# Performance work log

Hardware: AMD Instinct MI355X
Metric: run time of the kernel (lower is better)

Reference implementation:

```python
import jax, jax.numpy as jnp
import numpy as np

D = 2        # dof (input_dim of fc1)
H1 = 64      # hidden width
N = 262144   # batch
NEG_SLOPE = -0.01  # NOTE: original uses self.neg_slope=-0.01 in the analytic derivative
                   # while the forward activation uses F.leaky_relu default slope +0.01.
                   # We replicate this exactly.

def _lin_init(k, out_d, in_d):
    bound = 1.0 / np.sqrt(in_d)
    kw, kb = jax.random.split(k)
    W = jax.random.uniform(kw, (out_d, in_d), minval=-bound, maxval=bound, dtype=jnp.float32)
    b = jax.random.uniform(kb, (out_d,), minval=-bound, maxval=bound, dtype=jnp.float32)
    return W, b

def setup_inputs():
    key = jax.random.key(0)
    ks = jax.random.split(key, 6)
    W1, b1 = _lin_init(ks[0], H1, D)
    W1a, b1a = _lin_init(ks[1], H1, H1)
    W2, b2 = _lin_init(ks[2], D, H1)
    W3, b3 = _lin_init(ks[3], D, H1)
    W4, b4 = _lin_init(ks[4], 1, H1)
    x = jax.random.normal(ks[5], (N, 3 * D), dtype=jnp.float32)
    return {"x": x, "W1": W1, "b1": b1, "W1a": W1a, "b1a": b1a,
            "W2": W2, "b2": b2, "W3": W3, "b3": b3, "W4": W4, "b4": b4}

def _forward(x, W1, b1, W1a, b1a, W2, b2, W3, b3, W4, b4):
    n = x.shape[0]
    d = x.shape[1] // 3
    q, qd, qdd = x[:, :d], x[:, d:2 * d], x[:, 2 * d:]

    h1 = jax.nn.leaky_relu(q @ W1.T + b1, 0.01)       # [n,H1]
    h2 = jax.nn.leaky_relu(h1 @ W1a.T + b1a, 0.01)    # [n,H1]
    g = h2 @ W2.T + b2                                # [n,d]
    ld = jax.nn.relu(h2 @ W3.T + b3)                  # [n,d]  diagonal of L
    lo = h2 @ W4.T + b4                               # [n,1]  off-diagonal(s)

    # Analytic Jacobians. diag_embed(a) @ W == a[:,:,None] * W (no [n,H,H] materialization).
    dR1 = jnp.where(h1 > 0, 1.0, NEG_SLOPE)
    dh1_dq = dR1[:, :, None] * W1[None]                              # [n,H1,d]
    dR2 = jnp.where(h2 > 0, 1.0, NEG_SLOPE)
    dh2_dq = dR2[:, :, None] * jnp.einsum('hk,nkd->nhd', W1a, dh1_dq)  # [n,H1,d]
    dR3 = jnp.where(ld > 0, 1.0, 0.0)
    dld_dq = dR3[:, :, None] * jnp.einsum('oh,nhd->nod', W3, dh2_dq)   # [n,d,d]
    dlo_dq = jnp.einsum('oh,nhd->nod', W4, dh2_dq)                     # [n,1,d]

    dld_dqi = jnp.transpose(dld_dq, (0, 2, 1))[..., None]  # [n,d,d,1]
    dlo_dqi = jnp.transpose(dlo_dq, (0, 2, 1))[..., None]  # [n,d,1,1]
    dld_dt = dld_dq @ qd[:, :, None]                       # [n,d,1]
    dlo_dt = dlo_dq @ qd[:, :, None]                       # [n,1,1]

    zeros = jnp.zeros_like(ld)
    zeros2 = jnp.zeros_like(dld_dqi)
    Lc, dLt, dLq = [], [], []
    s, e = 0, d - 1
    for i in range(d):  # loop over d (=2) columns of the Cholesky factor
        Lc.append(jnp.concatenate([zeros[:, :i], ld[:, i:i + 1], lo[:, s:e]], axis=1))
        dLt.append(jnp.concatenate([zeros[:, :i], dld_dt[:, i].reshape(n, 1),
                                    dlo_dt[:, s:e].reshape(n, -1)], axis=1))
        dLq.append(jnp.concatenate([zeros2[:, :, :i].reshape(n, d, -1),
                                    dld_dqi[:, :, i].reshape(n, d, 1),
                                    dlo_dqi[:, :, s:e].reshape(n, d, -1)], axis=2))
        s, e = s + e, e + d - 2 - i
    L = jnp.stack(Lc, axis=2)                                    # [n,d,d]
    dL_dt = jnp.stack(dLt, axis=2)                               # [n,d,d]
    dL_dqi = jnp.transpose(jnp.stack(dLq, axis=3), (0, 2, 3, 1)) # [n,d,d,d]

    eps = 1e-5
    Lt = jnp.swapaxes(L, 1, 2)
    Hm = L @ Lt + eps * jnp.eye(d, dtype=x.dtype)
    dH_dt = L @ jnp.swapaxes(dL_dt, 1, 2) + dL_dt @ Lt

    qts = []
    for i in range(d):
        A = dL_dqi[..., i] @ Lt + L @ jnp.swapaxes(dL_dqi[..., i], 1, 2)
        qts.append(qd[:, None, :] @ A @ qd[:, :, None])  # [n,1,1]
    quad = jnp.stack(qts, axis=1).reshape(n, d, 1)

    c = dH_dt @ qd[:, :, None] - 0.5 * quad
    tau = Hm @ qdd[:, :, None] + c + g[:, :, None]
    return tau[..., 0], Hm, c[..., 0], g

def reference(x, W1, b1, W1a, b1a, W2, b2, W3, b3, W4, b4):
    return _forward(x, W1, b1, W1a, b1a, W2, b2, W3, b3, W4, b4)
```

## Files before the change

kernel.cpp:

```cpp
#include <hip/hip_runtime.h>
#include <stdint.h>


typedef __attribute__((ext_vector_type(8))) _Float16 f16x8;
typedef __attribute__((ext_vector_type(4))) float f32x4;
typedef __attribute__((ext_vector_type(2))) float f32x2;
typedef __attribute__((ext_vector_type(4))) unsigned int u32x4;

#define MFMA16(A,B,C) __builtin_amdgcn_mfma_f32_16x16x32_f16((A),(B),(C),0,0,0)

static __device__ __forceinline__ f32x2 pk_fma(f32x2 a, f32x2 b, f32x2 c) {
    f32x2 d;
    asm("v_pk_fma_f32 %0, %1, %2, %3" : "=v"(d) : "v"(a), "v"(b), "v"(c));
    return d;
}
static __device__ __forceinline__ f32x2 pk_mul(f32x2 a, f32x2 b) {
    f32x2 d;
    asm("v_pk_mul_f32 %0, %1, %2" : "=v"(d) : "v"(a), "v"(b));
    return d;
}
static __device__ __forceinline__ unsigned pkmul16(unsigned a, unsigned b) {
    unsigned d;
    asm("v_pk_mul_f16 %0, %1, %2" : "=v"(d) : "v"(a), "v"(b));
    return d;
}
static __device__ __forceinline__ float qsum(float v) {
    float a = v, b = v;
    asm("v_permlane16_swap_b32 %0, %1" : "+v"(a), "+v"(b));
    const float s = a + b;
    float c = s, d = s;
    asm("v_permlane32_swap_b32 %0, %1" : "+v"(c), "+v"(d));
    return c + d;
}

__global__ __launch_bounds__(256, 4) void delan_fwd(
    const float* __restrict__ x,
    const float* __restrict__ W1,  const float* __restrict__ b1,
    const float* __restrict__ W1a, const float* __restrict__ b1a,
    const float* __restrict__ W2,  const float* __restrict__ b2,
    const float* __restrict__ W3,  const float* __restrict__ b3,
    const float* __restrict__ W4,  const float* __restrict__ b4,
    float* __restrict__ out, int n_total)
{
    __shared__ _Float16 afrag[2][4][2][64][8];
    __shared__ float w0s[64], w1s[64], bs[64];
    __shared__ float cst[6][64];
    __shared__ unsigned scr[4][2][576];

    const int tid  = threadIdx.x;
    const int lane = tid & 63;
    const int wid  = tid >> 6;
    const int p    = lane & 15;
    const int qrt  = lane >> 4;

    if (tid < 64) {
        const int k = tid;
        w0s[k] = W1[2*k]; w1s[k] = W1[2*k+1]; bs[k] = b1[k];
        cst[0][k] = W2[k];      cst[1][k] = W2[64 + k];
        cst[2][k] = W3[k];      cst[3][k] = W3[64 + k];
        cst[4][k] = W4[k];      cst[5][k] = b1a[k];
    }
    {
        const int ht = wid;
#pragma unroll
        for (int kh = 0; kh < 2; ++kh) {
            const int row = ht * 16 + p;
            const int kb  = kh * 32 + qrt * 8;
            float wv[8];
            *(float4*)&wv[0] = *(const float4*)(W1a + row * 64 + kb);
            *(float4*)&wv[4] = *(const float4*)(W1a + row * 64 + kb + 4);
            f16x8 hi, lo;
#pragma unroll
            for (int j = 0; j < 8; ++j) {
                const _Float16 h = (_Float16)wv[j];
                hi[j] = h;
                lo[j] = (_Float16)((wv[j] - (float)h) * 4096.0f);
            }
            *(f16x8*)&afrag[0][ht][kh][lane][0] = hi;
            *(f16x8*)&afrag[1][ht][kh][lane][0] = lo;
        }
    }

    f16x8 A2[2];
    {
        const float* arow = (p == 0) ? W3 : (p == 1) ? (W3 + 64) : W4;
#pragma unroll
        for (int kh = 0; kh < 2; ++kh) {
            const int kb = kh * 32 + qrt * 8;
            const float4 aa = *(const float4*)(arow + kb);
            const float4 ab = *(const float4*)(arow + kb + 4);
            f16x8 f;
            f[0] = (_Float16)aa.x; f[1] = (_Float16)aa.y;
            f[2] = (_Float16)aa.z; f[3] = (_Float16)aa.w;
            f[4] = (_Float16)ab.x; f[5] = (_Float16)ab.y;
            f[6] = (_Float16)ab.z; f[7] = (_Float16)ab.w;
            if (p >= 3) {
#pragma unroll
                for (int j = 0; j < 8; ++j) f[j] = (_Float16)0.0f;
            }
            A2[kh] = f;
        }
    }
    __syncthreads();

    const f32x2 c4096  = {4096.0f, 4096.0f};
    const f32x2 cm4096 = {-4096.0f, -4096.0f};
    const long long N  = n_total;

#pragma unroll 1
    for (int t = 0; t < 4; ++t) {
        const int vb = blockIdx.x * 4 + t;
        const int s  = vb * 64 + wid * 16 + p;
        const int sc = (s < n_total) ? s : (n_total - 1);

        const float2 xa = *(const float2*)(x + 6 * sc);
        const float2 xb = *(const float2*)(x + 6 * sc + 2);
        const float2 xc = *(const float2*)(x + 6 * sc + 4);
        const float x0 = xa.x, x1 = xa.y;
        const float x2 = xb.x, x3 = xb.y;
        const float x4 = xc.x, x5 = xc.y;

        const f32x2 q00 = {x0, x0};
        const f32x2 q11 = {x1, x1};
        u32x4 Bhh[2], Bhl[2], Bu0[2], Bu1[2];
#pragma unroll
        for (int kh = 0; kh < 2; ++kh) {
            const int kb = kh * 32 + qrt * 8;
#pragma unroll
            for (int c = 0; c < 4; ++c) {
                const f32x2 w0p = *(const f32x2*)&w0s[kb + 2*c];
                const f32x2 w1p = *(const f32x2*)&w1s[kb + 2*c];
                const f32x2 bp  = *(const f32x2*)&bs [kb + 2*c];
                const f32x2 prep = pk_fma(w0p, q00, pk_fma(w1p, q11, bp));
                const bool pos0 = prep.x > 0.0f;
                const bool pos1 = prep.y > 0.0f;
                const unsigned mlo = pos0 ? 0x00003C00u : 0x0000A11Fu;
                const unsigned mhi = pos1 ? 0x3C000000u : 0xA11F0000u;
                const unsigned drw = mlo | mhi;
                const unsigned p0w = __builtin_bit_cast(unsigned,
                    __builtin_amdgcn_cvt_pkrtz(w0p.x, w0p.y));
                const unsigned p1w = __builtin_bit_cast(unsigned,
                    __builtin_amdgcn_cvt_pkrtz(w1p.x, w1p.y));
                Bu0[kh][c] = pkmul16(p0w, drw);
                Bu1[kh][c] = pkmul16(p1w, drw);
                f32x2 sp;
                sp.x = pos0 ? 1.0f : 0.01f;
                sp.y = pos1 ? 1.0f : 0.01f;
                const f32x2 h1p = pk_mul(prep, sp);
                const auto hhv = __builtin_amdgcn_cvt_pkrtz(h1p.x, h1p.y);
                Bhh[kh][c] = __builtin_bit_cast(unsigned, hhv);
                f32x2 hf;
                hf.x = (float)hhv[0];
                hf.y = (float)hhv[1];
                const f32x2 tt = pk_mul(h1p, c4096);
                const f32x2 rp = pk_fma(hf, cm4096, tt);
                Bhl[kh][c] = __builtin_bit_cast(unsigned,
                    __builtin_amdgcn_cvt_pkrtz(rp.x, rp.y));
            }
        }

        float ag0=0.f, ag1=0.f, al0=0.f, al1=0.f, aoo=0.f;
#pragma unroll
        for (int ht = 0; ht < 4; ++ht) {
            const f16x8 Ah0 = *(const f16x8*)&afrag[0][ht][0][lane][0];
            const f16x8 Ah1 = *(const f16x8*)&afrag[0][ht][1][lane][0];
            const f16x8 Al0 = *(const f16x8*)&afrag[1][ht][0][lane][0];
            const f16x8 Al1 = *(const f16x8*)&afrag[1][ht][1][lane][0];
            const f16x8 bh0 = __builtin_bit_cast(f16x8, Bhh[0]);
            const f16x8 bh1 = __builtin_bit_cast(f16x8, Bhh[1]);
            const f16x8 bl0 = __builtin_bit_cast(f16x8, Bhl[0]);
            const f16x8 bl1 = __builtin_bit_cast(f16x8, Bhl[1]);
            const f16x8 bu00 = __builtin_bit_cast(f16x8, Bu0[0]);
            const f16x8 bu01 = __builtin_bit_cast(f16x8, Bu0[1]);
            const f16x8 bu10 = __builtin_bit_cast(f16x8, Bu1[0]);
            const f16x8 bu11 = __builtin_bit_cast(f16x8, Bu1[1]);

            const int hb = ht * 16 + qrt * 4;
            f32x4 Chi = *(const f32x4*)&cst[5][hb];
            f32x4 Clo = {0.f,0.f,0.f,0.f};
            f32x4 Cz0 = {0.f,0.f,0.f,0.f};
            f32x4 Cz1 = {0.f,0.f,0.f,0.f};
            Chi = MFMA16(Ah0, bh0, Chi);  Chi = MFMA16(Ah1, bh1, Chi);
            Clo = MFMA16(Ah0, bl0, Clo);  Clo = MFMA16(Ah1, bl1, Clo);
            Clo = MFMA16(Al0, bh0, Clo);  Clo = MFMA16(Al1, bh1, Clo);
            Cz0 = MFMA16(Ah0, bu00, Cz0); Cz0 = MFMA16(Ah1, bu01, Cz0);
            Cz1 = MFMA16(Ah0, bu10, Cz1); Cz1 = MFMA16(Ah1, bu11, Cz1);

            const f32x4 w2a  = *(const f32x4*)&cst[0][hb];
            const f32x4 w2b  = *(const f32x4*)&cst[1][hb];
            const f32x4 w3a  = *(const f32x4*)&cst[2][hb];
            const f32x4 w3b  = *(const f32x4*)&cst[3][hb];
            const f32x4 w4v  = *(const f32x4*)&cst[4][hb];
            float d0v[4], d1v[4];
#pragma unroll
            for (int r = 0; r < 4; ++r) {
                const float ah = fmaf(2.44140625e-4f, Clo[r], Chi[r]);
                const bool pos = ah > 0.0f;
                const float h2 = pos ? ah : 0.01f * ah;
                ag0 = fmaf(w2a[r], h2, ag0);   ag1 = fmaf(w2b[r], h2, ag1);
                al0 = fmaf(w3a[r], h2, al0);   al1 = fmaf(w3b[r], h2, al1);
                aoo = fmaf(w4v[r], h2, aoo);
                d0v[r] = pos ? Cz0[r] : -0.01f * Cz0[r];
                d1v[r] = pos ? Cz1[r] : -0.01f * Cz1[r];
            }
            uint2 pk0, pk1;
            pk0.x = __builtin_bit_cast(unsigned,
                __builtin_amdgcn_cvt_pkrtz(d0v[0], d0v[1]));
            pk0.y = __builtin_bit_cast(unsigned,
                __builtin_amdgcn_cvt_pkrtz(d0v[2], d0v[3]));
            pk1.x = __builtin_bit_cast(unsigned,
                __builtin_amdgcn_cvt_pkrtz(d1v[0], d1v[1]));
            pk1.y = __builtin_bit_cast(unsigned,
                __builtin_amdgcn_cvt_pkrtz(d1v[2], d1v[3]));
            const int iw = p * 36 + 8 * ht + 2 * qrt;
            *(uint2*)&scr[wid][0][iw] = pk0;
            *(uint2*)&scr[wid][1][iw] = pk1;
        }

        const int ir = p * 36 + 4 * qrt;
        const f16x8 B00 = *(const f16x8*)&scr[wid][0][ir];
        const f16x8 B01 = *(const f16x8*)&scr[wid][0][ir + 16];
        const f16x8 B10 = *(const f16x8*)&scr[wid][1][ir];
        const f16x8 B11 = *(const f16x8*)&scr[wid][1][ir + 16];
        f32x4 Cd0 = {0.f,0.f,0.f,0.f};
        f32x4 Cd1 = {0.f,0.f,0.f,0.f};
        Cd0 = MFMA16(A2[0], B00, Cd0);  Cd0 = MFMA16(A2[1], B01, Cd0);
        Cd1 = MFMA16(A2[0], B10, Cd1);  Cd1 = MFMA16(A2[1], B11, Cd1);

        const float g0 = qsum(ag0) + b2[0];
        const float g1 = qsum(ag1) + b2[1];
        const float l0 = qsum(al0) + b3[0];
        const float l1 = qsum(al1) + b3[1];
        const float oo = qsum(aoo) + b4[0];
        const float p00 = Cd0[0], p10 = Cd0[1], r0 = Cd0[2];
        const float p01 = Cd1[0], p11 = Cd1[1], r1 = Cd1[2];

        const float ld0 = fmaxf(l0, 0.0f);
        const float ld1 = fmaxf(l1, 0.0f);
        const float dr30 = (l0 > 0.0f) ? 1.0f : 0.0f;
        const float dr31 = (l1 > 0.0f) ? 1.0f : 0.0f;

        const float da00 = dr30 * p00, da01 = dr30 * p01;
        const float da10 = dr31 * p10, da11 = dr31 * p11;

        const float l00 = ld0, l10 = oo, l11 = ld1;

        const float m00 = da00 * x2 + da01 * x3;
        const float m11 = da10 * x2 + da11 * x3;
        const float m10 = r0  * x2 + r1  * x3;

        const float eps = 1e-5f;
        const float Hm00 = fmaf(l00, l00, eps);
        const float Hm01 = l00 * l10;
        const float Hm11 = fmaf(l10, l10, fmaf(l11, l11, eps));

        const float dH00 = 2.0f * l00 * m00;
        const float dH01 = fmaf(l00, m10, l10 * m00);
        const float dH11 = 2.0f * fmaf(l10, m10, l11 * m11);

        const float x22 = x2 * x2, x23 = x2 * x3, x33 = x3 * x3;
        const float quad0 = 2.0f * (da00 * l00 * x22
                          + (fmaf(da00, l10, r0 * l00)) * x23
                          + (fmaf(r0, l10, da10 * l11)) * x33);
        const float quad1 = 2.0f * (da01 * l00 * x22
                          + (fmaf(da01, l10, r1 * l00)) * x23
                          + (fmaf(r1, l10, da11 * l11)) * x33);

        const float c0 = fmaf(dH00, x2, dH01 * x3) - 0.5f * quad0;
        const float c1 = fmaf(dH01, x2, dH11 * x3) - 0.5f * quad1;

        const float tau0 = fmaf(Hm00, x4, Hm01 * x5) + c0 + g0;
        const float tau1 = fmaf(Hm01, x4, Hm11 * x5) + c1 + g1;

        if (s < n_total && qrt == 0) {
            *((float2*)out + s)           = make_float2(tau0, tau1);
            *((float4*)(out + 2 * N) + s) = make_float4(Hm00, Hm01, Hm01, Hm11);
            *((float2*)(out + 6 * N) + s) = make_float2(c0, c1);
            *((float2*)(out + 8 * N) + s) = make_float2(g0, g1);
        }
    }
}

extern "C" void kernel_launch(void* const* d_in, const int* in_sizes, int n_in,
                              void* d_out, int out_size, void* d_ws, size_t ws_size,
                              hipStream_t stream) {
    const float* x   = (const float*)d_in[0];
    const float* W1  = (const float*)d_in[1];
    const float* b1  = (const float*)d_in[2];
    const float* W1a = (const float*)d_in[3];
    const float* b1a = (const float*)d_in[4];
    const float* W2  = (const float*)d_in[5];
    const float* b2  = (const float*)d_in[6];
    const float* W3  = (const float*)d_in[7];
    const float* b3  = (const float*)d_in[8];
    const float* W4  = (const float*)d_in[9];
    const float* b4  = (const float*)d_in[10];
    float* out = (float*)d_out;

    const int n_total = in_sizes[0] / 6;
    const int block = 256;
    const int grid = (n_total + 255) / 256;
    delan_fwd<<<grid, block, 0, stream>>>(x, W1, b1, W1a, b1a, W2, b2,
                                          W3, b3, W4, b4, out, n_total);
}
```

Measured before the change: 28.10 us.

## Move output-head reductions into MFMA and keep W1a hi fragments in registers

The g and off-diagonal output heads (W2, W4) are now computed by an extra MFMA over an fp16 h2 tile staged in shared scratch, replacing per-lane FMA accumulation and cross-lane reductions. Only the W3 reduction stays scalar. The high-part W1a fragments and b1a are held in registers instead of LDS, and W1/b1 are read directly from global memory. This cuts LDS traffic and VALU work but raises register pressure, adds fp16 rounding of h2 in the g and lo outputs, and introduces a lane-permute step to extract p10/p11.

```diff
diff --git a/kernel.cpp b/kernel.cpp
--- a/kernel.cpp
+++ b/kernel.cpp
@@ -6,6 +6,7 @@
 typedef __attribute__((ext_vector_type(4))) float f32x4;
 typedef __attribute__((ext_vector_type(2))) float f32x2;
 typedef __attribute__((ext_vector_type(4))) unsigned int u32x4;
+typedef __attribute__((ext_vector_type(2))) unsigned int u32x2;
 
 #define MFMA16(A,B,C) __builtin_amdgcn_mfma_f32_16x16x32_f16((A),(B),(C),0,0,0)
 
@@ -31,6 +32,19 @@
     float c = s, d = s;
     asm("v_permlane32_swap_b32 %0, %1" : "+v"(c), "+v"(d));
     return c + d;
+}
+static __device__ __forceinline__ float partner16(float v) {
+    float a = v, b = v;
+    asm("v_permlane16_swap_b32 %0, %1" : "+v"(a), "+v"(b));
+    return (a + b) - v;
+}
+static __device__ __forceinline__ f16x8 mk_f16x8(float4 a, float4 b) {
+    f16x8 f;
+    f[0] = (_Float16)a.x; f[1] = (_Float16)a.y;
+    f[2] = (_Float16)a.z; f[3] = (_Float16)a.w;
+    f[4] = (_Float16)b.x; f[5] = (_Float16)b.y;
+    f[6] = (_Float16)b.z; f[7] = (_Float16)b.w;
+    return f;
 }
 
 __global__ __launch_bounds__(256, 4) void delan_fwd(
@@ -42,10 +56,9 @@
     const float* __restrict__ W4,  const float* __restrict__ b4,
     float* __restrict__ out, int n_total)
 {
-    __shared__ _Float16 afrag[2][4][2][64][8];
-    __shared__ float w0s[64], w1s[64], bs[64];
-    __shared__ float cst[6][64];
-    __shared__ unsigned scr[4][2][576];
+    __shared__ _Float16 aflo[4][2][64][8];
+    __shared__ float w3s[2][64];
+    __shared__ unsigned scr[4][3][576];
 
     const int tid  = threadIdx.x;
     const int lane = tid & 63;
@@ -53,48 +66,44 @@
     const int p    = lane & 15;
     const int qrt  = lane >> 4;
 
-    if (tid < 64) {
-        const int k = tid;
-        w0s[k] = W1[2*k]; w1s[k] = W1[2*k+1]; bs[k] = b1[k];
-        cst[0][k] = W2[k];      cst[1][k] = W2[64 + k];
-        cst[2][k] = W3[k];      cst[3][k] = W3[64 + k];
-        cst[4][k] = W4[k];      cst[5][k] = b1a[k];
+    if (tid < 64) { w3s[0][tid] = W3[tid]; w3s[1][tid] = W3[64 + tid]; }
+
+    f16x8 Ah[4][2];
+#pragma unroll
+    for (int ht = 0; ht < 4; ++ht) {
+#pragma unroll
+        for (int kh = 0; kh < 2; ++kh) {
+            const float* src = W1a + (ht * 16 + p) * 64 + kh * 32 + qrt * 8;
+            const float4 a0 = *(const float4*)(src);
+            const float4 a1 = *(const float4*)(src + 4);
+            const float v[8] = {a0.x, a0.y, a0.z, a0.w, a1.x, a1.y, a1.z, a1.w};
+            f16x8 hi, lo;
+#pragma unroll
+            for (int j = 0; j < 8; ++j) {
+                const _Float16 h = (_Float16)v[j];
+                hi[j] = h;
+                lo[j] = (_Float16)((v[j] - (float)h) * 4096.0f);
+            }
+            Ah[ht][kh] = hi;
+            if (ht == wid) *(f16x8*)&aflo[ht][kh][lane][0] = lo;
+        }
     }
-    {
-        const int ht = wid;
-#pragma unroll
-        for (int kh = 0; kh < 2; ++kh) {
-            const int row = ht * 16 + p;
-            const int kb  = kh * 32 + qrt * 8;
-            float wv[8];
-            *(float4*)&wv[0] = *(const float4*)(W1a + row * 64 + kb);
-            *(float4*)&wv[4] = *(const float4*)(W1a + row * 64 + kb + 4);
-            f16x8 hi, lo;
-#pragma unroll
-            for (int j = 0; j < 8; ++j) {
-                const _Float16 h = (_Float16)wv[j];
-                hi[j] = h;
-                lo[j] = (_Float16)((wv[j] - (float)h) * 4096.0f);
-            }
-            *(f16x8*)&afrag[0][ht][kh][lane][0] = hi;
-            *(f16x8*)&afrag[1][ht][kh][lane][0] = lo;
-        }
-    }
+
+    f32x4 b1a_r[4];
+#pragma unroll
+    for (int ht = 0; ht < 4; ++ht)
+        b1a_r[ht] = *(const f32x4*)(b1a + ht * 16 + qrt * 4);
 
     f16x8 A2[2];
     {
-        const float* arow = (p == 0) ? W3 : (p == 1) ? (W3 + 64) : W4;
+        const float* arow = (p == 0) ? W2 : (p == 1) ? (W2 + 64)
+                          : (p == 2) ? W4 : (p == 3) ? W3 : (W3 + 64);
 #pragma unroll
         for (int kh = 0; kh < 2; ++kh) {
             const int kb = kh * 32 + qrt * 8;
-            const float4 aa = *(const float4*)(arow + kb);
-            const float4 ab = *(const float4*)(arow + kb + 4);
-            f16x8 f;
-            f[0] = (_Float16)aa.x; f[1] = (_Float16)aa.y;
-            f[2] = (_Float16)aa.z; f[3] = (_Float16)aa.w;
-            f[4] = (_Float16)ab.x; f[5] = (_Float16)ab.y;
-            f[6] = (_Float16)ab.z; f[7] = (_Float16)ab.w;
-            if (p >= 3) {
+            f16x8 f = mk_f16x8(*(const float4*)(arow + kb),
+                               *(const float4*)(arow + kb + 4));
+            if (p >= 5) {
 #pragma unroll
                 for (int j = 0; j < 8; ++j) f[j] = (_Float16)0.0f;
             }
@@ -109,8 +118,7 @@
 
 #pragma unroll 1
     for (int t = 0; t < 4; ++t) {
-        const int vb = blockIdx.x * 4 + t;
-        const int s  = vb * 64 + wid * 16 + p;
+        const int s  = (blockIdx.x * 4 + t) * 64 + wid * 16 + p;
         const int sc = (s < n_total) ? s : (n_total - 1);
 
         const float2 xa = *(const float2*)(x + 6 * sc);
@@ -126,11 +134,17 @@
 #pragma unroll
         for (int kh = 0; kh < 2; ++kh) {
             const int kb = kh * 32 + qrt * 8;
+            const float4* wq = (const float4*)(W1 + 2 * kb);
+            const float4 bq0 = *(const float4*)(b1 + kb);
+            const float4 bq1 = *(const float4*)(b1 + kb + 4);
+            const float bv[8] = {bq0.x, bq0.y, bq0.z, bq0.w,
+                                 bq1.x, bq1.y, bq1.z, bq1.w};
 #pragma unroll
             for (int c = 0; c < 4; ++c) {
-                const f32x2 w0p = *(const f32x2*)&w0s[kb + 2*c];
-                const f32x2 w1p = *(const f32x2*)&w1s[kb + 2*c];
-                const f32x2 bp  = *(const f32x2*)&bs [kb + 2*c];
+                const float4 w = wq[c];
+                const f32x2 w0p = {w.x, w.z};
+                const f32x2 w1p = {w.y, w.w};
+                const f32x2 bp  = {bv[2*c], bv[2*c+1]};
                 const f32x2 prep = pk_fma(w0p, q00, pk_fma(w1p, q11, bp));
                 const bool pos0 = prep.x > 0.0f;
                 const bool pos1 = prep.y > 0.0f;
@@ -159,13 +173,13 @@
             }
         }
 
-        float ag0=0.f, ag1=0.f, al0=0.f, al1=0.f, aoo=0.f;
+        float al0 = 0.f, al1 = 0.f;
 #pragma unroll
         for (int ht = 0; ht < 4; ++ht) {
-            const f16x8 Ah0 = *(const f16x8*)&afrag[0][ht][0][lane][0];
-            const f16x8 Ah1 = *(const f16x8*)&afrag[0][ht][1][lane][0];
-            const f16x8 Al0 = *(const f16x8*)&afrag[1][ht][0][lane][0];
-            const f16x8 Al1 = *(const f16x8*)&afrag[1][ht][1][lane][0];
+            const f16x8 Ah0 = Ah[ht][0];
+            const f16x8 Ah1 = Ah[ht][1];
+            const f16x8 Al0 = *(const f16x8*)&aflo[ht][0][lane][0];
+            const f16x8 Al1 = *(const f16x8*)&aflo[ht][1][lane][0];
             const f16x8 bh0 = __builtin_bit_cast(f16x8, Bhh[0]);
             const f16x8 bh1 = __builtin_bit_cast(f16x8, Bhh[1]);
             const f16x8 bl0 = __builtin_bit_cast(f16x8, Bhl[0]);
@@ -175,8 +189,7 @@
             const f16x8 bu10 = __builtin_bit_cast(f16x8, Bu1[0]);
             const f16x8 bu11 = __builtin_bit_cast(f16x8, Bu1[1]);
 
-            const int hb = ht * 16 + qrt * 4;
-            f32x4 Chi = *(const f32x4*)&cst[5][hb];
+            f32x4 Chi = b1a_r[ht];
             f32x4 Clo = {0.f,0.f,0.f,0.f};
             f32x4 Cz0 = {0.f,0.f,0.f,0.f};
             f32x4 Cz1 = {0.f,0.f,0.f,0.f};
@@ -186,54 +199,56 @@
             Cz0 = MFMA16(Ah0, bu00, Cz0); Cz0 = MFMA16(Ah1, bu01, Cz0);
             Cz1 = MFMA16(Ah0, bu10, Cz1); Cz1 = MFMA16(Ah1, bu11, Cz1);
 
-            const f32x4 w2a  = *(const f32x4*)&cst[0][hb];
-            const f32x4 w2b  = *(const f32x4*)&cst[1][hb];
-            const f32x4 w3a  = *(const f32x4*)&cst[2][hb];
-            const f32x4 w3b  = *(const f32x4*)&cst[3][hb];
-            const f32x4 w4v  = *(const f32x4*)&cst[4][hb];
-            float d0v[4], d1v[4];
+            const f32x4 w3a = *(const f32x4*)&w3s[0][ht * 16 + qrt * 4];
+            const f32x4 w3b = *(const f32x4*)&w3s[1][ht * 16 + qrt * 4];
+            float h2v[4], d0v[4], d1v[4];
 #pragma unroll
             for (int r = 0; r < 4; ++r) {
                 const float ah = fmaf(2.44140625e-4f, Clo[r], Chi[r]);
                 const bool pos = ah > 0.0f;
                 const float h2 = pos ? ah : 0.01f * ah;
-                ag0 = fmaf(w2a[r], h2, ag0);   ag1 = fmaf(w2b[r], h2, ag1);
-                al0 = fmaf(w3a[r], h2, al0);   al1 = fmaf(w3b[r], h2, al1);
-                aoo = fmaf(w4v[r], h2, aoo);
+                h2v[r] = h2;
+                al0 = fmaf(w3a[r], h2, al0);
+                al1 = fmaf(w3b[r], h2, al1);
                 d0v[r] = pos ? Cz0[r] : -0.01f * Cz0[r];
                 d1v[r] = pos ? Cz1[r] : -0.01f * Cz1[r];
             }
-            uint2 pk0, pk1;
-            pk0.x = __builtin_bit_cast(unsigned,
-                __builtin_amdgcn_cvt_pkrtz(d0v[0], d0v[1]));
-            pk0.y = __builtin_bit_cast(unsigned,
-                __builtin_amdgcn_cvt_pkrtz(d0v[2], d0v[3]));
-            pk1.x = __builtin_bit_cast(unsigned,
-                __builtin_amdgcn_cvt_pkrtz(d1v[0], d1v[1]));
-            pk1.y = __builtin_bit_cast(unsigned,
-                __builtin_amdgcn_cvt_pkrtz(d1v[2], d1v[3]));
+            u32x2 ph, pd0, pd1;
+            ph[0]  = __builtin_bit_cast(unsigned, __builtin_amdgcn_cvt_pkrtz(h2v[0], h2v[1]));
+            ph[1]  = __builtin_bit_cast(unsigned, __builtin_amdgcn_cvt_pkrtz(h2v[2], h2v[3]));
+            pd0[0] = __builtin_bit_cast(unsigned, __builtin_amdgcn_cvt_pkrtz(d0v[0], d0v[1]));
+            pd0[1] = __builtin_bit_cast(unsigned, __builtin_amdgcn_cvt_pkrtz(d0v[2], d0v[3]));
+            pd1[0] = __builtin_bit_cast(unsigned, __builtin_amdgcn_cvt_pkrtz(d1v[0], d1v[1]));
+            pd1[1] = __builtin_bit_cast(unsigned, __builtin_amdgcn_cvt_pkrtz(d1v[2], d1v[3]));
             const int iw = p * 36 + 8 * ht + 2 * qrt;
-            *(uint2*)&scr[wid][0][iw] = pk0;
-            *(uint2*)&scr[wid][1][iw] = pk1;
+            *(u32x2*)&scr[wid][0][iw] = ph;
+            *(u32x2*)&scr[wid][1][iw] = pd0;
+            *(u32x2*)&scr[wid][2][iw] = pd1;
         }
 
         const int ir = p * 36 + 4 * qrt;
-        const f16x8 B00 = *(const f16x8*)&scr[wid][0][ir];
-        const f16x8 B01 = *(const f16x8*)&scr[wid][0][ir + 16];
-        const f16x8 B10 = *(const f16x8*)&scr[wid][1][ir];
-        const f16x8 B11 = *(const f16x8*)&scr[wid][1][ir + 16];
+        const f16x8 Bh2a = *(const f16x8*)&scr[wid][0][ir];
+        const f16x8 Bh2b = *(const f16x8*)&scr[wid][0][ir + 16];
+        const f16x8 Bd0a = *(const f16x8*)&scr[wid][1][ir];
+        const f16x8 Bd0b = *(const f16x8*)&scr[wid][1][ir + 16];
+        const f16x8 Bd1a = *(const f16x8*)&scr[wid][2][ir];
+        const f16x8 Bd1b = *(const f16x8*)&scr[wid][2][ir + 16];
+        f32x4 Ch  = {0.f,0.f,0.f,0.f};
         f32x4 Cd0 = {0.f,0.f,0.f,0.f};
         f32x4 Cd1 = {0.f,0.f,0.f,0.f};
-        Cd0 = MFMA16(A2[0], B00, Cd0);  Cd0 = MFMA16(A2[1], B01, Cd0);
-        Cd1 = MFMA16(A2[0], B10, Cd1);  Cd1 = MFMA16(A2[1], B11, Cd1);
-
-        const float g0 = qsum(ag0) + b2[0];
-        const float g1 = qsum(ag1) + b2[1];
+        Ch  = MFMA16(A2[0], Bh2a, Ch);   Ch  = MFMA16(A2[1], Bh2b, Ch);
+        Cd0 = MFMA16(A2[0], Bd0a, Cd0);  Cd0 = MFMA16(A2[1], Bd0b, Cd0);
+        Cd1 = MFMA16(A2[0], Bd1a, Cd1);  Cd1 = MFMA16(A2[1], Bd1b, Cd1);
+
+        const float g0 = Ch[0] + b2[0];
+        const float g1 = Ch[1] + b2[1];
+        const float oo = Ch[2] + b4[0];
+        const float r0 = Cd0[2], p00 = Cd0[3];
+        const float r1 = Cd1[2], p01 = Cd1[3];
+        const float p10 = partner16(Cd0[0]);
+        const float p11 = partner16(Cd1[0]);
         const float l0 = qsum(al0) + b3[0];
         const float l1 = qsum(al1) + b3[1];
-        const float oo = qsum(aoo) + b4[0];
-        const float p00 = Cd0[0], p10 = Cd0[1], r0 = Cd0[2];
-        const float p01 = Cd1[0], p11 = Cd1[1], r1 = Cd1[2];
 
         const float ld0 = fmaxf(l0, 0.0f);
         const float ld1 = fmaxf(l1, 0.0f);
```

Result: slower. 48.95 us (+74.2%).
